# Optimization experiments

Measured on AMD Instinct MI355X. Metric: run time of the kernel, lower is better.

## Reference

```python
import math
import jax, jax.numpy as jnp
import numpy as np

B, L, DIM, HEADS = 4, 2048, 1024, 8
HEAD = DIM // HEADS  # 128
SCALE_BASE = 512.0
EPS = 1e-5  # nn.GroupNorm default


def _xpos(x, downscale=False):
    # x: (..., L, dh). Faithful port of the RetNet XPOS (Jamie-Stirling impl).
    l, dh = x.shape[-2], x.shape[-1]
    half = dh // 2
    pos = jnp.arange(l, dtype=x.dtype)
    base = (jnp.arange(0, dh, 2, dtype=x.dtype) + 0.4 * dh) / (1.4 * dh)  # (half,)
    scale = base[None, :] ** (pos[:, None] / SCALE_BASE)                  # (L, half)
    inv_freq = 1.0 / (10000.0 ** (jnp.arange(half, dtype=x.dtype) / half))
    sinusoid = pos[:, None] * inv_freq[None, :]                           # (L, half)
    sin, cos = jnp.sin(sinusoid), jnp.cos(sinusoid)
    if downscale:
        scale = 1.0 / scale
    s = jnp.repeat(sin * scale, 2, axis=-1)  # duplicate_interleave -> (L, dh)
    c = jnp.repeat(cos * scale, 2, axis=-1)
    x1, x2 = x[..., ::2], x[..., 1::2]
    rot = jnp.stack([-x2, x1], axis=-1).reshape(x.shape)  # rotate_every_two
    return x * c + rot * s


def _decay_mask(l, gammas):
    # D[h, n, m] = gamma_h ** (n - m) for n >= m else 0
    n = jnp.arange(l)[:, None]
    m = jnp.arange(l)[None, :]
    lg = jnp.log(gammas)  # (h,)
    expo = (n - m).astype(jnp.float32)[None, :, :] * lg[:, None, None]
    return jnp.where((n >= m)[None], jnp.exp(expo), 0.0)  # (h, L, L)


def setup_inputs() -> dict:
    key = jax.random.key(0)
    ks = jax.random.split(key, 6)
    d = DIM
    return {
        "X": jax.random.normal(ks[0], (B, L, DIM), dtype=jnp.float32),
        "W_Q": jax.random.normal(ks[1], (HEADS, DIM, HEAD), dtype=jnp.float32) / d,
        "W_K": jax.random.normal(ks[2], (HEADS, DIM, HEAD), dtype=jnp.float32) / d,
        "W_V": jax.random.normal(ks[3], (HEADS, DIM, HEAD), dtype=jnp.float32) / d,
        "W_G": jax.random.normal(ks[4], (DIM, DIM), dtype=jnp.float32) / d,
        "W_O": jax.random.normal(ks[5], (DIM, DIM), dtype=jnp.float32) / d,
        "gn_weight": jnp.ones((DIM,), dtype=jnp.float32),
        "gn_bias": jnp.zeros((DIM,), dtype=jnp.float32),
    }


def reference(X, W_Q, W_K, W_V, W_G, W_O, gn_weight, gn_bias):
    b, l, d = X.shape
    h = W_Q.shape[0]
    # gammas = 1 - exp(linspace(log 1/32, log 1/512, heads))
    gammas = 1.0 - jnp.exp(jnp.linspace(math.log(1.0 / 32.0), math.log(1.0 / 512.0), h)).astype(jnp.float32)

    Q = jnp.einsum('bld,hde->bhle', X, W_Q)
    K = jnp.einsum('bld,hde->bhle', X, W_K)
    V = jnp.einsum('bld,hdv->bhlv', X, W_V)
    Q = _xpos(Q)
    K = _xpos(K, downscale=True)

    D = _decay_mask(l, gammas).astype(X.dtype)           # (h, L, L)
    scores = jnp.einsum('bhle,bhme->bhlm', Q, K) * D[None]
    Y = jnp.einsum('bhlm,bhmv->bhlv', scores, V)          # (b, h, L, head_v)

    # GroupNorm(heads, V) on rows of shape (V,): normalize per head group
    mean = Y.mean(axis=-1, keepdims=True)
    var = Y.var(axis=-1, keepdims=True)
    Yn = (Y - mean) * jax.lax.rsqrt(var + EPS)
    Yn = jnp.transpose(Yn, (0, 2, 1, 3)).reshape(b, l, -1)  # concat heads -> (b, L, V)
    Yn = Yn * gn_weight + gn_bias

    G = X @ W_G
    out = (G * jax.nn.sigmoid(G) * Yn) @ W_O  # swish gate then output proj
    return out
```

## Files before the change

kernel.cpp:

```cpp
#include <hip/hip_runtime.h>
#include <cmath>

#define BB 4
#define LL 2048
#define DD 1024
#define HH 8
#define MM (BB * LL)

struct Gammas { float lg2[8]; };
struct MMArgs { const ushort* Bt[4]; void* C[4]; void* C2[4]; int emode[4]; };

typedef __attribute__((ext_vector_type(8))) short bf16x8;
typedef __attribute__((ext_vector_type(4))) float f32x4;

__device__ __forceinline__ ushort f2bf(float f) {
    uint u = __builtin_bit_cast(uint, f);
    uint r = (u + 0x7fffu + ((u >> 16) & 1u)) >> 16;
    return (ushort)r;
}
__device__ __forceinline__ float bf2f(ushort h) {
    uint u = ((uint)h) << 16;
    return __builtin_bit_cast(float, u);
}
__device__ __forceinline__ void gload16(const void* g, void* l) {
    __builtin_amdgcn_global_load_lds((const __attribute__((address_space(1))) void*)g,
                                     (__attribute__((address_space(3))) void*)l, 16, 0, 0);
}

__global__ void xpos_table_kernel(float4* __restrict__ tbl) {
    int tid = blockIdx.x * blockDim.x + threadIdx.x;
    if (tid >= LL * 64) return;
    int l = tid >> 6, i = tid & 63;
    float inv = powf(10000.0f, -(float)i / 64.0f);
    float ang = (float)l * inv;
    float s = sinf(ang), c = cosf(ang);
    float base = (2.0f * (float)i + 51.2f) / 179.2f;
    float sc = powf(base, (float)l / 512.0f);
    tbl[tid] = make_float4(c * sc, s * sc, c / sc, s / sc);
}

__global__ __launch_bounds__(256) void cast_kernel(const float* __restrict__ X,
                                                   ushort* __restrict__ Xb) {
    int i = (blockIdx.x * 256 + threadIdx.x) * 4;
    float4 v = *(const float4*)&X[i];
    ushort4 o;
    o.x = f2bf(v.x); o.y = f2bf(v.y); o.z = f2bf(v.z); o.w = f2bf(v.w);
    *(ushort4*)&Xb[i] = o;
}

__global__ __launch_bounds__(256) void wtrans_kernel(const float* __restrict__ W,
                                                     ushort* __restrict__ Wt, int perhead) {
    __shared__ float T[64][68];
    const int k0 = blockIdx.y * 64, n0 = blockIdx.x * 64;
    const int t = threadIdx.x;
    for (int f = t; f < 64 * 16; f += 256) {
        int kk = f >> 4, s = f & 15;
        int n = n0 + s * 4;
        size_t src = perhead ? (size_t)(n >> 7) * 131072 + (size_t)(k0 + kk) * 128 + (n & 127)
                             : (size_t)(k0 + kk) * 1024 + n;
        *(float4*)&T[kk][s * 4] = *(const float4*)&W[src];
    }
    __syncthreads();
    for (int f = t; f < 64 * 8; f += 256) {
        int n = f >> 3, s = f & 7;
        __align__(16) ushort tmp[8];
        #pragma unroll
        for (int j = 0; j < 8; j++) tmp[j] = f2bf(T[s * 8 + j][n]);
        *(uint4*)&Wt[(size_t)(n0 + n) * 1024 + k0 + s * 8] = *(uint4*)tmp;
    }
}

__global__ __launch_bounds__(256) void mm_kernel(
    const ushort* __restrict__ A, MMArgs args, const float4* __restrict__ tbl)
{
    __shared__ __align__(16) ushort As[2][128 * 32];
    __shared__ __align__(16) ushort Bs[2][128 * 32];
    const int t = threadIdx.x;
    const int w = t >> 6, lane = t & 63;
    const int ln = lane & 15, quad = lane >> 4;
    const int which = blockIdx.x >> 3;
    const ushort* Bt = args.Bt[which];
    void* Cv = args.C[which];
    void* Cv2 = args.C2[which];
    const int emode = args.emode[which];
    const int n0 = (blockIdx.x & 7) * 128, m0 = blockIdx.y * 128;
    const int wm = w & 1, wn = w >> 1;

    f32x4 acc[4][4];
    const f32x4 fzero = {0.f, 0.f, 0.f, 0.f};
    #pragma unroll
    for (int i = 0; i < 4; i++)
        #pragma unroll
        for (int j = 0; j < 4; j++) acc[i][j] = fzero;

    const int srow = w * 32 + (lane >> 2);
    const int scol = (lane & 3) * 8;
    const ushort* ga  = A  + (size_t)(m0 + srow) * 1024 + scol;
    const ushort* ga2 = ga + 16 * 1024;
    const ushort* gb  = Bt + (size_t)(n0 + srow) * 1024 + scol;
    const ushort* gb2 = gb + 16 * 1024;
    const int lo1 = (w * 32) * 32;
    const int lo2 = (w * 32 + 16) * 32;

    gload16(ga, &As[0][lo1]);
    gload16(ga2, &As[0][lo2]);
    gload16(gb, &Bs[0][lo1]);
    gload16(gb2, &Bs[0][lo2]);
    __syncthreads();

    for (int kt = 0; kt < 1024; kt += 32) {
        const int cur = (kt >> 5) & 1;
        if (kt < 1024 - 32) {
            const int nk = kt + 32;
            gload16(ga + nk, &As[cur ^ 1][lo1]);
            gload16(ga2 + nk, &As[cur ^ 1][lo2]);
            gload16(gb + nk, &Bs[cur ^ 1][lo1]);
            gload16(gb2 + nk, &Bs[cur ^ 1][lo2]);
        }
        bf16x8 am[4], bn[4];
        #pragma unroll
        for (int i = 0; i < 4; i++)
            am[i] = *(const bf16x8*)&As[cur][(wm * 64 + i * 16 + ln) * 32 + quad * 8];
        #pragma unroll
        for (int i = 0; i < 4; i++)
            bn[i] = *(const bf16x8*)&Bs[cur][(wn * 64 + i * 16 + ln) * 32 + quad * 8];
        #pragma unroll
        for (int mi = 0; mi < 4; mi++)
            #pragma unroll
            for (int ni = 0; ni < 4; ni++)
                acc[mi][ni] = __builtin_amdgcn_mfma_f32_16x16x32_bf16(
                    am[mi], bn[ni], acc[mi][ni], 0, 0, 0);
        __syncthreads();
    }

    #pragma unroll
    for (int mi = 0; mi < 4; mi++) {
        #pragma unroll
        for (int ni = 0; ni < 4; ni++) {
            const int row0 = m0 + wm * 64 + mi * 16 + quad * 4;
            const int e = wn * 64 + ni * 16 + ln;
            const int col = n0 + e;
            if (emode == 5) {
                const int b = row0 >> 11, l0 = row0 & (LL - 1);
                ushort4 pk;
                pk.x = f2bf(acc[mi][ni][0]); pk.y = f2bf(acc[mi][ni][1]);
                pk.z = f2bf(acc[mi][ni][2]); pk.w = f2bf(acc[mi][ni][3]);
                *(ushort4*)&((ushort*)Cv)[((size_t)(b * 1024 + col)) * 2048 + l0] = pk;
                continue;
            }
            float vv[4];
            #pragma unroll
            for (int r = 0; r < 4; r++) {
                float v = acc[mi][ni][r];
                if (emode == 1 || emode == 2 || emode == 6) {
                    float4 tt = tbl[(size_t)((row0 + r) & (LL - 1)) * 64 + (e >> 1)];
                    float cc = (emode == 1) ? tt.x : tt.z;
                    float ss = (emode == 1) ? tt.y : tt.w;
                    float partner = __shfl_xor(v, 1);
                    float rot = (e & 1) ? partner : -partner;
                    v = v * cc + rot * ss;
                } else if (emode == 3) {
                    v = v / (1.0f + expf(-v));
                }
                vv[r] = v;
                if (emode == 4)
                    ((float*)Cv)[(size_t)(row0 + r) * 1024 + col] = v;
                else
                    ((ushort*)Cv)[(size_t)(row0 + r) * 1024 + col] = f2bf(v);
            }
            if (emode == 6) {
                const int b = row0 >> 11, l0 = row0 & (LL - 1);
                ushort4 pk;
                pk.x = f2bf(vv[0]); pk.y = f2bf(vv[1]);
                pk.z = f2bf(vv[2]); pk.w = f2bf(vv[3]);
                *(ushort4*)&((ushort*)Cv2)[((size_t)(b * 1024 + col)) * 2048 + l0] = pk;
            }
        }
    }
}

__global__ __launch_bounds__(256) void state_kernel(
    const ushort* __restrict__ Ktb, const ushort* __restrict__ Vt,
    ushort* __restrict__ Sb, Gammas gp)
{
    __shared__ __align__(16) ushort shbuf[2 * 128 * 72];
    ushort* Ktl = shbuf;
    ushort* Vwl = shbuf + 128 * 72;

    const int t = threadIdx.x;
    const int w = t >> 6, lane = t & 63, ln = lane & 15, quad = lane >> 4;
    const int c = blockIdx.x, bh = blockIdx.y;
    const int b = bh >> 3, h = bh & 7;
    const float lg2 = gp.lg2[h];
    const size_t tbase = ((size_t)b * 1024 + h * 128) * 2048 + (size_t)c * 64;

    const int sr = t >> 1, soff = (t & 1) * 32;
    #pragma unroll
    for (int j = 0; j < 4; j++)
        *(uint4*)&Ktl[sr * 72 + soff + j * 8] =
            *(const uint4*)&Ktb[tbase + (size_t)sr * 2048 + soff + j * 8];
    #pragma unroll
    for (int j = 0; j < 4; j++) {
        uint4 raw = *(const uint4*)&Vt[tbase + (size_t)sr * 2048 + soff + j * 8];
        ushort* rp = (ushort*)&raw;
        __align__(16) ushort tmp[8];
        #pragma unroll
        for (int jj = 0; jj < 8; jj++) {
            int m = soff + j * 8 + jj;
            tmp[jj] = f2bf(bf2f(rp[jj]) * exp2f(lg2 * (float)(63 - m)));
        }
        *(uint4*)&Vwl[sr * 72 + soff + j * 8] = *(uint4*)tmp;
    }
    __syncthreads();

    const int wm = w & 1, wn = w >> 1;
    f32x4 acc[4][4];
    const f32x4 fzero = {0.f, 0.f, 0.f, 0.f};
    #pragma unroll
    for (int i = 0; i < 4; i++)
        #pragma unroll
        for (int j = 0; j < 4; j++) acc[i][j] = fzero;

    #pragma unroll
    for (int ks = 0; ks < 2; ks++) {
        bf16x8 am[4], bn[4];
        #pragma unroll
        for (int mi = 0; mi < 4; mi++)
            am[mi] = *(const bf16x8*)&Ktl[(wm * 64 + mi * 16 + ln) * 72 + ks * 32 + quad * 8];
        #pragma unroll
        for (int ni = 0; ni < 4; ni++)
            bn[ni] = *(const bf16x8*)&Vwl[(wn * 64 + ni * 16 + ln) * 72 + ks * 32 + quad * 8];
        #pragma unroll
        for (int mi = 0; mi < 4; mi++)
            #pragma unroll
            for (int ni = 0; ni < 4; ni++)
                acc[mi][ni] = __builtin_amdgcn_mfma_f32_16x16x32_bf16(
                    am[mi], bn[ni], acc[mi][ni], 0, 0, 0);
    }
    __syncthreads();

    ushort* Lsh = shbuf;
    #pragma unroll
    for (int mi = 0; mi < 4; mi++) {
        #pragma unroll
        for (int ni = 0; ni < 4; ni++) {
            const int d0 = wm * 64 + mi * 16 + quad * 4;
            const int v = wn * 64 + ni * 16 + ln;
            ushort4 pk;
            pk.x = f2bf(acc[mi][ni][0]); pk.y = f2bf(acc[mi][ni][1]);
            pk.z = f2bf(acc[mi][ni][2]); pk.w = f2bf(acc[mi][ni][3]);
            *(ushort4*)&Lsh[v * 136 + d0] = pk;
        }
    }
    __syncthreads();
    ushort* dst = Sb + (size_t)(bh * 32 + c) * 128 * 128;
    const int orow = t >> 1, ooff = (t & 1) * 64;
    #pragma unroll
    for (int j = 0; j < 8; j++)
        *(uint4*)&dst[(size_t)orow * 128 + ooff + j * 8] =
            *(uint4*)&Lsh[orow * 136 + ooff + j * 8];
}

__global__ __launch_bounds__(256) void scan_kernel(ushort* __restrict__ Sb, Gammas gp)
{
    const int t = threadIdx.x;
    const int vb = blockIdx.x, bh = blockIdx.y;
    const int h = bh & 7;
    const float g64 = exp2f(64.0f * gp.lg2[h]);
    const int v = vb * 16 + (t >> 4);
    const int d0 = (t & 15) * 8;

    float acc[8];
    #pragma unroll
    for (int j = 0; j < 8; j++) acc[j] = 0.f;

    for (int c = 1; c < 32; c++) {
        ushort* p = Sb + ((size_t)(bh * 32 + (c - 1)) * 128 + v) * 128 + d0;
        uint4 lv = *(const uint4*)p;
        ushort* lp = (ushort*)&lv;
        __align__(16) ushort o[8];
        #pragma unroll
        for (int j = 0; j < 8; j++) {
            acc[j] = g64 * acc[j] + bf2f(lp[j]);
            o[j] = f2bf(acc[j]);
        }
        *(uint4*)p = *(uint4*)o;
    }
}

__global__ __launch_bounds__(256) void ret2_kernel(
    const ushort* __restrict__ Qb, const ushort* __restrict__ Kb,
    const ushort* __restrict__ Vt, const ushort* __restrict__ Pt,
    const ushort* __restrict__ Gb,
    const float* __restrict__ gnw, const float* __restrict__ gnb,
    ushort* __restrict__ Z, Gammas gp)
{
    __shared__ __align__(16) ushort Ks[64 * 136];
    __shared__ __align__(16) ushort Vs[128 * 72];
    __shared__ __align__(16) ushort Ss[64 * 72];
    __shared__ __align__(16) ushort Ps[128 * 136];

    const int t = threadIdx.x;
    const int w = t >> 6, lane = t & 63, ln = lane & 15, quad = lane >> 4;
    const int c = blockIdx.x, bh = blockIdx.y;
    const int b = bh >> 3, h = bh & 7;
    const float lg2 = gp.lg2[h];
    const size_t qkbase = (size_t)b * LL * 1024 + (size_t)h * 128;
    const size_t vtbase = ((size_t)b * 1024 + h * 128) * 2048;
    const int n0 = c * 64;

    float dmk[4], drr[4];
    #pragma unroll
    for (int kt = 0; kt < 4; kt++)
        dmk[kt] = exp2f(-(float)(kt * 16 + quad * 4) * lg2);
    #pragma unroll
    for (int r = 0; r < 4; r++)
        drr[r] = exp2f(-(float)r * lg2);

    float gwv[8], gbv[8];
    #pragma unroll
    for (int vt = 0; vt < 8; vt++) {
        gwv[vt] = gnw[h * 128 + vt * 16 + ln];
        gbv[vt] = gnb[h * 128 + vt * 16 + ln];
    }

    const int krow = t >> 4, kc = (t & 15) * 8;
    const int vrow = t >> 3, vc = (t & 7) * 8;
    #pragma unroll
    for (int i = 0; i < 4; i++)
        *(uint4*)&Ks[(krow + i * 16) * 136 + kc] =
            *(const uint4*)&Kb[qkbase + (size_t)(n0 + krow + i * 16) * 1024 + kc];
    #pragma unroll
    for (int i = 0; i < 4; i++)
        *(uint4*)&Vs[(vrow + i * 32) * 72 + vc] =
            *(const uint4*)&Vt[vtbase + (size_t)(vrow + i * 32) * 2048 + n0 + vc];
    if (c > 0) {
        const ushort* psrc = Pt + (size_t)(bh * 32 + (c - 1)) * 128 * 128;
        const int pr = t >> 1, poff = (t & 1) * 64;
        #pragma unroll
        for (int j = 0; j < 8; j++)
            *(uint4*)&Ps[pr * 136 + poff + j * 8] =
                *(const uint4*)&psrc[(size_t)pr * 128 + poff + j * 8];
    }

    bf16x8 aq[4];
    #pragma unroll
    for (int ks = 0; ks < 4; ks++)
        aq[ks] = *(const bf16x8*)&Qb[qkbase + (size_t)(n0 + 16 * w + ln) * 1024
                                     + ks * 32 + quad * 8];
    f32x4 y[8];
    const f32x4 fzero = {0.f, 0.f, 0.f, 0.f};
    #pragma unroll
    for (int vt = 0; vt < 8; vt++) y[vt] = fzero;

    __syncthreads();

    if (c > 0) {
        #pragma unroll
        for (int ks = 0; ks < 4; ks++) {
            #pragma unroll
            for (int vt = 0; vt < 8; vt++) {
                bf16x8 bp = *(const bf16x8*)&Ps[(vt * 16 + ln) * 136 + ks * 32 + quad * 8];
                y[vt] = __builtin_amdgcn_mfma_f32_16x16x32_bf16(aq[ks], bp, y[vt], 0, 0, 0);
            }
        }
        #pragma unroll
        for (int rr = 0; rr < 4; rr++) {
            const float sc = exp2f(lg2 * (float)(16 * w + quad * 4 + rr + 1));
            #pragma unroll
            for (int vt = 0; vt < 8; vt++) y[vt][rr] *= sc;
        }
    }

    f32x4 s4[4];
    #pragma unroll
    for (int kt = 0; kt < 4; kt++) s4[kt] = fzero;
    #pragma unroll
    for (int ks = 0; ks < 4; ks++) {
        #pragma unroll
        for (int kt = 0; kt < 4; kt++) {
            bf16x8 bk = *(const bf16x8*)&Ks[(kt * 16 + ln) * 136 + ks * 32 + quad * 8];
            s4[kt] = __builtin_amdgcn_mfma_f32_16x16x32_bf16(bk, aq[ks], s4[kt], 0, 0, 0);
        }
    }
    const float dq = exp2f((float)(16 * w + ln) * lg2);
    #pragma unroll
    for (int kt = 0; kt < 4; kt++) {
        const float db = dq * dmk[kt];
        ushort4 pk;
        pk.x = f2bf((kt * 16 + quad * 4 + 0 <= 16 * w + ln) ? s4[kt][0] * db * drr[0] : 0.f);
        pk.y = f2bf((kt * 16 + quad * 4 + 1 <= 16 * w + ln) ? s4[kt][1] * db * drr[1] : 0.f);
        pk.z = f2bf((kt * 16 + quad * 4 + 2 <= 16 * w + ln) ? s4[kt][2] * db * drr[2] : 0.f);
        pk.w = f2bf((kt * 16 + quad * 4 + 3 <= 16 * w + ln) ? s4[kt][3] * db * drr[3] : 0.f);
        *(ushort4*)&Ss[(16 * w + ln) * 72 + kt * 16 + quad * 4] = pk;
    }
    #pragma unroll
    for (int ks2 = 0; ks2 < 2; ks2++) {
        bf16x8 as = *(const bf16x8*)&Ss[(16 * w + ln) * 72 + ks2 * 32 + quad * 8];
        #pragma unroll
        for (int vt = 0; vt < 8; vt++) {
            bf16x8 bv = *(const bf16x8*)&Vs[(vt * 16 + ln) * 72 + ks2 * 32 + quad * 8];
            y[vt] = __builtin_amdgcn_mfma_f32_16x16x32_bf16(as, bv, y[vt], 0, 0, 0);
        }
    }

    #pragma unroll
    for (int r = 0; r < 4; r++) {
        float s = 0.f, sq = 0.f;
        #pragma unroll
        for (int vt = 0; vt < 8; vt++) {
            float v = y[vt][r];
            s += v; sq += v * v;
        }
        #pragma unroll
        for (int off = 8; off >= 1; off >>= 1) {
            s  += __shfl_xor(s, off, 64);
            sq += __shfl_xor(sq, off, 64);
        }
        float mean = s * 0.0078125f;
        float var = sq * 0.0078125f - mean * mean;
        float rstd = rsqrtf(var + 1e-5f);
        const size_t row = (size_t)(b * LL + n0 + 16 * w + quad * 4 + r);
        #pragma unroll
        for (int vt = 0; vt < 8; vt++) {
            float gv = bf2f(Gb[row * 1024 + h * 128 + vt * 16 + ln]);
            float o = (y[vt][r] - mean) * rstd * gwv[vt] + gbv[vt];
            Z[row * 1024 + h * 128 + vt * 16 + ln] = f2bf(o * gv);
        }
    }
}

extern "C" void kernel_launch(void* const* d_in, const int* in_sizes, int n_in,
                              void* d_out, int out_size, void* d_ws, size_t ws_size,
                              hipStream_t stream) {
    const float* X   = (const float*)d_in[0];
    const float* Wq  = (const float*)d_in[1];
    const float* Wk  = (const float*)d_in[2];
    const float* Wv  = (const float*)d_in[3];
    const float* Wg  = (const float*)d_in[4];
    const float* Wo  = (const float*)d_in[5];
    const float* gnw = (const float*)d_in[6];
    const float* gnb = (const float*)d_in[7];
    float* out = (float*)d_out;

    const size_t MB = 1u << 20;
    char* base = (char*)d_ws;
    ushort* Sb  = (ushort*)base;
    float4* tbl = (float4*)base;
    ushort* Xb  = (ushort*)(base + 2 * MB);
    ushort* Wqt = (ushort*)(base + 18 * MB);
    ushort* Wkt = (ushort*)(base + 20 * MB);
    ushort* Wvt = (ushort*)(base + 22 * MB);
    ushort* Wgt = (ushort*)(base + 24 * MB);
    ushort* Wot = (ushort*)(base + 32 * MB);
    ushort* Qb  = (ushort*)(base + 34 * MB);
    ushort* Kb  = (ushort*)(base + 50 * MB);
    ushort* Gb  = (ushort*)(base + 66 * MB);
    ushort* Vt  = (ushort*)(base + 82 * MB);
    ushort* Ktb = (ushort*)(base + 98 * MB);
    ushort* Zb  = (ushort*)(base + 98 * MB);

    Gammas gp;
    for (int h = 0; h < 8; h++) {
        double lin = log(1.0 / 32.0) +
                     (log(1.0 / 512.0) - log(1.0 / 32.0)) * (double)h / 7.0;
        float gamma = 1.0f - expf((float)lin);
        gp.lg2[h] = log2f(gamma);
    }

    xpos_table_kernel<<<(LL * 64) / 256, 256, 0, stream>>>(tbl);
    cast_kernel<<<MM * 1024 / 1024, 256, 0, stream>>>(X, Xb);

    dim3 wgrid(16, 16);
    wtrans_kernel<<<wgrid, 256, 0, stream>>>(Wq, Wqt, 1);
    wtrans_kernel<<<wgrid, 256, 0, stream>>>(Wk, Wkt, 1);
    wtrans_kernel<<<wgrid, 256, 0, stream>>>(Wv, Wvt, 1);
    wtrans_kernel<<<wgrid, 256, 0, stream>>>(Wg, Wgt, 0);
    wtrans_kernel<<<wgrid, 256, 0, stream>>>(Wo, Wot, 0);

    MMArgs qa;
    qa.Bt[0] = Wqt; qa.Bt[1] = Wkt; qa.Bt[2] = Wvt; qa.Bt[3] = Wgt;
    qa.C[0] = Qb;   qa.C[1] = Kb;   qa.C[2] = Vt;   qa.C[3] = Gb;
    qa.C2[0] = nullptr; qa.C2[1] = Ktb; qa.C2[2] = nullptr; qa.C2[3] = nullptr;
    qa.emode[0] = 1; qa.emode[1] = 6; qa.emode[2] = 5; qa.emode[3] = 3;
    mm_kernel<<<dim3(32, 64), 256, 0, stream>>>(Xb, qa, tbl);

    state_kernel<<<dim3(32, 32), 256, 0, stream>>>(Ktb, Vt, Sb, gp);
    scan_kernel<<<dim3(8, 32), 256, 0, stream>>>(Sb, gp);
    ret2_kernel<<<dim3(32, 32), 256, 0, stream>>>(Qb, Kb, Vt, Sb, Gb,
                                                  gnw, gnb, Zb, gp);

    MMArgs oa;
    oa.Bt[0] = Wot; oa.Bt[1] = Wot; oa.Bt[2] = Wot; oa.Bt[3] = Wot;
    oa.C[0] = out;  oa.C[1] = out;  oa.C[2] = out;  oa.C[3] = out;
    oa.C2[0] = nullptr; oa.C2[1] = nullptr; oa.C2[2] = nullptr; oa.C2[3] = nullptr;
    oa.emode[0] = 4; oa.emode[1] = 4; oa.emode[2] = 4; oa.emode[3] = 4;
    mm_kernel<<<dim3(8, 64), 256, 0, stream>>>(Zb, oa, tbl);
}
```

Before: 394.1 us.

## Use 256x256-tile 8-wave GEMM with 4-stage LDS pipeline for QKVG projection

Replaces the fused Q/K/V/G projection GEMM with a new 512-thread kernel computing 256x256 output tiles. It uses a 4-deep LDS buffer ring with two tiles in flight, explicit vmcnt waits, split barriers, s_setprio around the MFMA blocks, and an XOR-swizzled LDS layout to avoid bank conflicts. The aim is more reuse per loaded tile and better overlap of global loads with MFMA. The larger tile uses more registers and LDS and leaves fewer workgroups (512) to fill the GPU. The old kernel is kept, stripped of the xpos epilogue paths, for the output projection.

```diff
diff --git a/kernel.cpp b/kernel.cpp
--- a/kernel.cpp
+++ b/kernel.cpp
@@ -70,74 +70,110 @@
     }
 }
 
-__global__ __launch_bounds__(256) void mm_kernel(
+#define MM8_STEP(T, STAGE, VM)                                                  \
+  {                                                                             \
+    const int buf_ = (T) & 3;                                                   \
+    const int sbuf_ = ((T) + 2) & 3;                                            \
+    if (STAGE) {                                                                \
+      const int nk_ = ((T) + 2) * 32;                                           \
+      gload16(gA0 + nk_, &As[sbuf_][ldst]);                                     \
+      gload16(gA1 + nk_, &As[sbuf_][4096 + ldst]);                              \
+    }                                                                           \
+    asm volatile("s_waitcnt vmcnt(" #VM ")" ::: "memory");                      \
+    __builtin_amdgcn_sched_barrier(0);                                          \
+    __builtin_amdgcn_s_barrier();                                               \
+    __builtin_amdgcn_sched_barrier(0);                                          \
+    bf16x8 am[8], bn[4];                                                        \
+    _Pragma("unroll")                                                           \
+    for (int mi = 0; mi < 4; mi++)                                              \
+      am[mi] = *(const bf16x8*)&As[buf_][aoff + mi * 512];                      \
+    _Pragma("unroll")                                                           \
+    for (int ni = 0; ni < 4; ni++)                                              \
+      bn[ni] = *(const bf16x8*)&Bs[buf_][boff + ni * 512];                      \
+    __builtin_amdgcn_s_setprio(1);                                              \
+    _Pragma("unroll")                                                           \
+    for (int mi = 0; mi < 4; mi++)                                              \
+      _Pragma("unroll")                                                         \
+      for (int ni = 0; ni < 4; ni++)                                            \
+        acc[mi][ni] = __builtin_amdgcn_mfma_f32_16x16x32_bf16(                  \
+            am[mi], bn[ni], acc[mi][ni], 0, 0, 0);                              \
+    __builtin_amdgcn_s_setprio(0);                                              \
+    __builtin_amdgcn_sched_barrier(0);                                          \
+    if (STAGE) {                                                                \
+      const int nk_ = ((T) + 2) * 32;                                           \
+      gload16(gB0 + nk_, &Bs[sbuf_][ldst]);                                     \
+      gload16(gB1 + nk_, &Bs[sbuf_][4096 + ldst]);                              \
+    }                                                                           \
+    __builtin_amdgcn_sched_barrier(0);                                          \
+    __builtin_amdgcn_s_barrier();                                               \
+    __builtin_amdgcn_sched_barrier(0);                                          \
+    _Pragma("unroll")                                                           \
+    for (int mi = 4; mi < 8; mi++)                                              \
+      am[mi] = *(const bf16x8*)&As[buf_][aoff + mi * 512];                      \
+    __builtin_amdgcn_s_setprio(1);                                              \
+    _Pragma("unroll")                                                           \
+    for (int mi = 4; mi < 8; mi++)                                              \
+      _Pragma("unroll")                                                         \
+      for (int ni = 0; ni < 4; ni++)                                            \
+        acc[mi][ni] = __builtin_amdgcn_mfma_f32_16x16x32_bf16(                  \
+            am[mi], bn[ni], acc[mi][ni], 0, 0, 0);                              \
+    __builtin_amdgcn_s_setprio(0);                                              \
+  }
+
+__global__ __launch_bounds__(512) void mm8_kernel(
     const ushort* __restrict__ A, MMArgs args, const float4* __restrict__ tbl)
 {
-    __shared__ __align__(16) ushort As[2][128 * 32];
-    __shared__ __align__(16) ushort Bs[2][128 * 32];
+    __shared__ __align__(16) ushort As[4][8192];
+    __shared__ __align__(16) ushort Bs[4][8192];
     const int t = threadIdx.x;
     const int w = t >> 6, lane = t & 63;
     const int ln = lane & 15, quad = lane >> 4;
-    const int which = blockIdx.x >> 3;
+    const int which = blockIdx.x >> 2;
     const ushort* Bt = args.Bt[which];
     void* Cv = args.C[which];
     void* Cv2 = args.C2[which];
     const int emode = args.emode[which];
-    const int n0 = (blockIdx.x & 7) * 128, m0 = blockIdx.y * 128;
+    const int n0 = (blockIdx.x & 3) * 256, m0 = blockIdx.y * 256;
     const int wm = w & 1, wn = w >> 1;
 
-    f32x4 acc[4][4];
+    f32x4 acc[8][4];
     const f32x4 fzero = {0.f, 0.f, 0.f, 0.f};
     #pragma unroll
-    for (int i = 0; i < 4; i++)
+    for (int i = 0; i < 8; i++)
         #pragma unroll
         for (int j = 0; j < 4; j++) acc[i][j] = fzero;
 
-    const int srow = w * 32 + (lane >> 2);
-    const int scol = (lane & 3) * 8;
-    const ushort* ga  = A  + (size_t)(m0 + srow) * 1024 + scol;
-    const ushort* ga2 = ga + 16 * 1024;
-    const ushort* gb  = Bt + (size_t)(n0 + srow) * 1024 + scol;
-    const ushort* gb2 = gb + 16 * 1024;
-    const int lo1 = (w * 32) * 32;
-    const int lo2 = (w * 32 + 16) * 32;
-
-    gload16(ga, &As[0][lo1]);
-    gload16(ga2, &As[0][lo2]);
-    gload16(gb, &Bs[0][lo1]);
-    gload16(gb2, &Bs[0][lo2]);
-    __syncthreads();
-
-    for (int kt = 0; kt < 1024; kt += 32) {
-        const int cur = (kt >> 5) & 1;
-        if (kt < 1024 - 32) {
-            const int nk = kt + 32;
-            gload16(ga + nk, &As[cur ^ 1][lo1]);
-            gload16(ga2 + nk, &As[cur ^ 1][lo2]);
-            gload16(gb + nk, &Bs[cur ^ 1][lo1]);
-            gload16(gb2 + nk, &Bs[cur ^ 1][lo2]);
-        }
-        bf16x8 am[4], bn[4];
-        #pragma unroll
-        for (int i = 0; i < 4; i++)
-            am[i] = *(const bf16x8*)&As[cur][(wm * 64 + i * 16 + ln) * 32 + quad * 8];
-        #pragma unroll
-        for (int i = 0; i < 4; i++)
-            bn[i] = *(const bf16x8*)&Bs[cur][(wn * 64 + i * 16 + ln) * 32 + quad * 8];
-        #pragma unroll
-        for (int mi = 0; mi < 4; mi++)
-            #pragma unroll
-            for (int ni = 0; ni < 4; ni++)
-                acc[mi][ni] = __builtin_amdgcn_mfma_f32_16x16x32_bf16(
-                    am[mi], bn[ni], acc[mi][ni], 0, 0, 0);
-        __syncthreads();
-    }
-
-    #pragma unroll
-    for (int mi = 0; mi < 4; mi++) {
+    const int srow = w * 16 + (lane >> 2);
+    const int scol = ((lane & 3) ^ ((lane >> 3) & 3)) * 8;
+    const ushort* gA0 = A  + (size_t)(m0 + srow) * 1024 + scol;
+    const ushort* gA1 = gA0 + (size_t)128 * 1024;
+    const ushort* gB0 = Bt + (size_t)(n0 + srow) * 1024 + scol;
+    const ushort* gB1 = gB0 + (size_t)128 * 1024;
+    const int ldst = w * 512;
+
+    const int cQ = (quad ^ ((ln >> 1) & 3)) * 8;
+    const int aoff = (wm * 128 + ln) * 32 + cQ;
+    const int boff = (wn * 64 + ln) * 32 + cQ;
+
+    #pragma unroll
+    for (int tt = 0; tt < 2; ++tt) {
+        gload16(gA0 + tt * 32, &As[tt][ldst]);
+        gload16(gA1 + tt * 32, &As[tt][4096 + ldst]);
+        gload16(gB0 + tt * 32, &Bs[tt][ldst]);
+        gload16(gB1 + tt * 32, &Bs[tt][4096 + ldst]);
+    }
+
+    for (int T = 0; T < 30; ++T) {
+        MM8_STEP(T, 1, 6);
+    }
+    MM8_STEP(30, 0, 4);
+    MM8_STEP(31, 0, 0);
+
+    #pragma unroll
+    for (int mi = 0; mi < 8; mi++) {
         #pragma unroll
         for (int ni = 0; ni < 4; ni++) {
-            const int row0 = m0 + wm * 64 + mi * 16 + quad * 4;
+            const int row0 = m0 + wm * 128 + mi * 16 + quad * 4;
             const int e = wn * 64 + ni * 16 + ln;
             const int col = n0 + e;
             if (emode == 5) {
@@ -153,11 +189,11 @@
             for (int r = 0; r < 4; r++) {
                 float v = acc[mi][ni][r];
                 if (emode == 1 || emode == 2 || emode == 6) {
-                    float4 tt = tbl[(size_t)((row0 + r) & (LL - 1)) * 64 + (e >> 1)];
+                    float4 tt = tbl[(size_t)((row0 + r) & (LL - 1)) * 64 + ((col & 127) >> 1)];
                     float cc = (emode == 1) ? tt.x : tt.z;
                     float ss = (emode == 1) ? tt.y : tt.w;
                     float partner = __shfl_xor(v, 1);
-                    float rot = (e & 1) ? partner : -partner;
+                    float rot = (col & 1) ? partner : -partner;
                     v = v * cc + rot * ss;
                 } else if (emode == 3) {
                     v = v / (1.0f + expf(-v));
@@ -179,6 +215,88 @@
     }
 }
 
+__global__ __launch_bounds__(256) void mm_kernel(
+    const ushort* __restrict__ A, MMArgs args, const float4* __restrict__ tbl)
+{
+    __shared__ __align__(16) ushort As[2][128 * 32];
+    __shared__ __align__(16) ushort Bs[2][128 * 32];
+    const int t = threadIdx.x;
+    const int w = t >> 6, lane = t & 63;
+    const int ln = lane & 15, quad = lane >> 4;
+    const int which = blockIdx.x >> 3;
+    const ushort* Bt = args.Bt[which];
+    void* Cv = args.C[which];
+    const int emode = args.emode[which];
+    const int n0 = (blockIdx.x & 7) * 128, m0 = blockIdx.y * 128;
+    const int wm = w & 1, wn = w >> 1;
+
+    f32x4 acc[4][4];
+    const f32x4 fzero = {0.f, 0.f, 0.f, 0.f};
+    #pragma unroll
+    for (int i = 0; i < 4; i++)
+        #pragma unroll
+        for (int j = 0; j < 4; j++) acc[i][j] = fzero;
+
+    const int srow = w * 32 + (lane >> 2);
+    const int scol = (lane & 3) * 8;
+    const ushort* ga  = A  + (size_t)(m0 + srow) * 1024 + scol;
+    const ushort* ga2 = ga + 16 * 1024;
+    const ushort* gb  = Bt + (size_t)(n0 + srow) * 1024 + scol;
+    const ushort* gb2 = gb + 16 * 1024;
+    const int lo1 = (w * 32) * 32;
+    const int lo2 = (w * 32 + 16) * 32;
+
+    gload16(ga, &As[0][lo1]);
+    gload16(ga2, &As[0][lo2]);
+    gload16(gb, &Bs[0][lo1]);
+    gload16(gb2, &Bs[0][lo2]);
+    __syncthreads();
+
+    for (int kt = 0; kt < 1024; kt += 32) {
+        const int cur = (kt >> 5) & 1;
+        if (kt < 1024 - 32) {
+            const int nk = kt + 32;
+            gload16(ga + nk, &As[cur ^ 1][lo1]);
+            gload16(ga2 + nk, &As[cur ^ 1][lo2]);
+            gload16(gb + nk, &Bs[cur ^ 1][lo1]);
+            gload16(gb2 + nk, &Bs[cur ^ 1][lo2]);
+        }
+        bf16x8 am[4], bn[4];
+        #pragma unroll
+        for (int i = 0; i < 4; i++)
+            am[i] = *(const bf16x8*)&As[cur][(wm * 64 + i * 16 + ln) * 32 + quad * 8];
+        #pragma unroll
+        for (int i = 0; i < 4; i++)
+            bn[i] = *(const bf16x8*)&Bs[cur][(wn * 64 + i * 16 + ln) * 32 + quad * 8];
+        #pragma unroll
+        for (int mi = 0; mi < 4; mi++)
+            #pragma unroll
+            for (int ni = 0; ni < 4; ni++)
+                acc[mi][ni] = __builtin_amdgcn_mfma_f32_16x16x32_bf16(
+                    am[mi], bn[ni], acc[mi][ni], 0, 0, 0);
+        __syncthreads();
+    }
+
+    #pragma unroll
+    for (int mi = 0; mi < 4; mi++) {
+        #pragma unroll
+        for (int ni = 0; ni < 4; ni++) {
+            const int row0 = m0 + wm * 64 + mi * 16 + quad * 4;
+            const int e = wn * 64 + ni * 16 + ln;
+            const int col = n0 + e;
+            #pragma unroll
+            for (int r = 0; r < 4; r++) {
+                float v = acc[mi][ni][r];
+                if (emode == 3) v = v / (1.0f + expf(-v));
+                if (emode == 4)
+                    ((float*)Cv)[(size_t)(row0 + r) * 1024 + col] = v;
+                else
+                    ((ushort*)Cv)[(size_t)(row0 + r) * 1024 + col] = f2bf(v);
+            }
+        }
+    }
+}
+
 __global__ __launch_bounds__(256) void state_kernel(
     const ushort* __restrict__ Ktb, const ushort* __restrict__ Vt,
     ushort* __restrict__ Sb, Gammas gp)
@@ -483,7 +601,7 @@
     qa.C[0] = Qb;   qa.C[1] = Kb;   qa.C[2] = Vt;   qa.C[3] = Gb;
     qa.C2[0] = nullptr; qa.C2[1] = Ktb; qa.C2[2] = nullptr; qa.C2[3] = nullptr;
     qa.emode[0] = 1; qa.emode[1] = 6; qa.emode[2] = 5; qa.emode[3] = 3;
-    mm_kernel<<<dim3(32, 64), 256, 0, stream>>>(Xb, qa, tbl);
+    mm8_kernel<<<dim3(16, 32), 512, 0, stream>>>(Xb, qa, tbl);
 
     state_kernel<<<dim3(32, 32), 256, 0, stream>>>(Ktb, Vt, Sb, gp);
     scan_kernel<<<dim3(8, 32), 256, 0, stream>>>(Sb, gp);
```

After: 404.5 us. 2.6% more time.
